# Performance work log

Measured on AMD Instinct MI355X. Metric: run time of the kernel, lower is better.

Reference implementation:

```python
import jax, jax.numpy as jnp
import numpy as np

N_HEAD = 16

def setup_inputs() -> dict:
    key = jax.random.key(0)
    ks = jax.random.split(key, 5)
    B, T, C = 8, 1024, 1024
    s = 0.02
    return {
        "x": jax.random.normal(ks[0], (B, T, C), jnp.float32),
        "W_qkv": jax.random.normal(ks[1], (C, 3 * C), jnp.float32) * s,
        "b_qkv": jnp.zeros((3 * C,), jnp.float32),
        "W_proj": jax.random.normal(ks[2], (C, C), jnp.float32) * s,
        "b_proj": jnp.zeros((C,), jnp.float32),
    }

def reference(x, W_qkv, b_qkv, W_proj, b_proj):
    B, T, C = x.shape
    H = N_HEAD
    hs = C // H
    qkv = x @ W_qkv + b_qkv                       # [B,T,3C]
    q, k, v = jnp.split(qkv, 3, axis=-1)
    # [B,T,C] -> [B,H,T,hs]
    q = q.reshape(B, T, H, hs).transpose(0, 2, 1, 3)
    k = k.reshape(B, T, H, hs).transpose(0, 2, 1, 3)
    v = v.reshape(B, T, H, hs).transpose(0, 2, 1, 3)
    scores = jnp.einsum('bhqd,bhkd->bhqk', q, k) * (hs ** -0.5)  # [B,H,T,T]
    causal = jnp.tril(jnp.ones((T, T), dtype=bool))
    scores = jnp.where(causal[None, None], scores, jnp.finfo(scores.dtype).min)
    attn = jax.nn.softmax(scores, axis=-1)
    # dropout layers are identity in eval mode
    out = jnp.einsum('bhqk,bhkd->bhqd', attn, v)  # [B,H,T,hs]
    out = out.transpose(0, 2, 1, 3).reshape(B, T, C)
    return out @ W_proj + b_proj
```

## Files before the change

### kernel.cpp

```cpp
#include <hip/hip_runtime.h>

#define TT 1024
#define CC 1024
#define NH 16
#define HS 64

typedef __attribute__((ext_vector_type(8))) short short8;
typedef __attribute__((ext_vector_type(4))) float f32x4;

__device__ inline unsigned short f2bf(float f) {
  unsigned int u = __float_as_uint(f);
  unsigned int r = u + 0x7FFFu + ((u >> 16) & 1u);
  return (unsigned short)(r >> 16);
}

__device__ inline unsigned int cvtpk_bf16(float lo, float hi) {
  unsigned int r;
  asm("v_cvt_pk_bf16_f32 %0, %1, %2" : "=v"(r) : "v"(lo), "v"(hi));
  return r;
}

#define GLDS16(g, l)                                                         \
  __builtin_amdgcn_global_load_lds(                                          \
      (const __attribute__((address_space(1))) void*)(g),                    \
      (__attribute__((address_space(3))) void*)(l), 16, 0, 0)

__global__ __launch_bounds__(256) void f32_to_bf16(
    const float* __restrict__ in, unsigned short* __restrict__ out, int n4) {
  int i = (blockIdx.x * 256 + threadIdx.x);
  if (i >= n4) return;
  float4 v = *(const float4*)&in[(size_t)i * 4];
  ushort4 o;
  o.x = f2bf(v.x); o.y = f2bf(v.y); o.z = f2bf(v.z); o.w = f2bf(v.w);
  *(ushort4*)&out[(size_t)i * 4] = o;
}

__global__ __launch_bounds__(256) void transpose_to_bf16(
    const float* __restrict__ W, unsigned short* __restrict__ Wt,
    int K, int N) {
  __shared__ float tile[32][33];
  const int n0 = blockIdx.x * 32, k0 = blockIdx.y * 32;
  const int t = threadIdx.x;
  {
    const int kr = t >> 3;
    const int nc = (t & 7) * 4;
    float4 v = *(const float4*)&W[(size_t)(k0 + kr) * N + n0 + nc];
    tile[kr][nc + 0] = v.x; tile[kr][nc + 1] = v.y;
    tile[kr][nc + 2] = v.z; tile[kr][nc + 3] = v.w;
  }
  __syncthreads();
  {
    const int nr = t >> 3;
    const int kc = (t & 7) * 4;
    ushort4 o;
    o.x = f2bf(tile[kc + 0][nr]);
    o.y = f2bf(tile[kc + 1][nr]);
    o.z = f2bf(tile[kc + 2][nr]);
    o.w = f2bf(tile[kc + 3][nr]);
    *(ushort4*)&Wt[(size_t)(n0 + nr) * K + k0 + kc] = o;
  }
}

template <bool BF16_OUT>
__global__ __launch_bounds__(256) void gemm_bt_mfma(
    const unsigned short* __restrict__ A,
    const unsigned short* __restrict__ Bt,
    const float* __restrict__ bias,
    void* __restrict__ Cv,
    int M, int N, int K) {
  __shared__ __attribute__((aligned(16))) unsigned short As[128 * 32];
  __shared__ __attribute__((aligned(16))) unsigned short Bs[128 * 32];

  const int tid = threadIdx.x;
  const int w = tid >> 6;
  const int l = tid & 63;
  const int wm = w >> 1, wn = w & 1;

  const int brow = blockIdx.y * 128;
  const int bcol = blockIdx.x * 128;

  const int srow = w * 32 + (l >> 2);
  const int skoff = (l & 3) * 8;
  const unsigned short* Ag = A + (size_t)(brow + srow) * K + skoff;
  const unsigned short* Bg = Bt + (size_t)(bcol + srow) * K + skoff;

  typedef __attribute__((address_space(3))) unsigned short lds_us;
  lds_us* AsW = (lds_us*)As + w * 1024;
  lds_us* BsW = (lds_us*)Bs + w * 1024;

  f32x4 acc[4][4] = {};

  const int fr = l & 15;
  const int fk = (l >> 4) * 8;

  const int nk = K >> 5;
  for (int kt = 0; kt < nk; ++kt) {
    const unsigned short* ag = Ag + kt * 32;
    const unsigned short* bg = Bg + kt * 32;
    GLDS16(ag,          AsW);
    GLDS16(ag + 16 * K, AsW + 512);
    GLDS16(bg,          BsW);
    GLDS16(bg + 16 * K, BsW + 512);
    __syncthreads();

    short8 af[4], bfr[4];
#pragma unroll
    for (int m = 0; m < 4; ++m)
      af[m] = *(const short8*)&As[(wm * 64 + m * 16 + fr) * 32 + fk];
#pragma unroll
    for (int n = 0; n < 4; ++n)
      bfr[n] = *(const short8*)&Bs[(wn * 64 + n * 16 + fr) * 32 + fk];
#pragma unroll
    for (int m = 0; m < 4; ++m)
#pragma unroll
      for (int n = 0; n < 4; ++n)
        acc[m][n] = __builtin_amdgcn_mfma_f32_16x16x32_bf16(
            af[m], bfr[n], acc[m][n], 0, 0, 0);
    __syncthreads();
  }

#pragma unroll
  for (int n = 0; n < 4; ++n) {
    const int col = bcol + wn * 64 + n * 16 + fr;
    const float bv = bias[col];
#pragma unroll
    for (int m = 0; m < 4; ++m) {
      const int row0 = brow + wm * 64 + m * 16 + (l >> 4) * 4;
#pragma unroll
      for (int j = 0; j < 4; ++j) {
        const float val = acc[m][n][j] + bv;
        if (BF16_OUT)
          ((unsigned short*)Cv)[(size_t)(row0 + j) * N + col] = f2bf(val);
        else
          ((float*)Cv)[(size_t)(row0 + j) * N + col] = val;
      }
    }
  }
}

#define C1 0.18033688f

__global__ __launch_bounds__(256) void attn_mfma(
    const unsigned short* __restrict__ qkv, unsigned short* __restrict__ aout) {
  const int bh = blockIdx.y;
  const int b = bh >> 4, h = bh & 15;
  const int tid = threadIdx.x;
  const int w = tid >> 6;
  const int l = tid & 63;
  const int lr = l & 15;
  const int lg = l >> 4;

  __shared__ __attribute__((aligned(16))) unsigned short Kl[64 * 64];
  __shared__ __attribute__((aligned(16))) unsigned short Vt[64 * 64];
  __shared__ __attribute__((aligned(16))) unsigned short Pq[4][32 * 64];

  const size_t row3c = 3 * CC;
  const unsigned short* qbase = qkv + (size_t)(b * TT) * row3c + h * HS;
  const unsigned short* kbase = qbase + CC;
  const unsigned short* vbase = qbase + 2 * CC;

  const int ksrow = 16 * w + (l >> 3);
  const int ksbyte = (((l & 7) ^ (l >> 3)) << 4);
  typedef __attribute__((address_space(3))) unsigned short lds_us;
  lds_us* KlW0 = (lds_us*)Kl + (16 * w) * 64;
  lds_us* KlW1 = (lds_us*)Kl + (16 * w + 8) * 64;

#pragma unroll 1
  for (int pass = 0; pass < 2; ++pass) {
    const int qt = pass ? (7 - blockIdx.x) : blockIdx.x;
    const int qw = qt * 128 + w * 32;

    short8 aq[2][2];
#pragma unroll
    for (int mi = 0; mi < 2; ++mi)
#pragma unroll
      for (int ks = 0; ks < 2; ++ks)
        aq[mi][ks] = *(const short8*)(qbase +
            (size_t)(qw + mi * 16 + lr) * row3c + ks * 32 + lg * 8);

    f32x4 sOT[4][2] = {};
    float lpart[2] = {0.f, 0.f};

    const int ntiles = 2 * qt + 2;
    for (int kt = 0; kt < ntiles; ++kt) {
      const int k0 = kt * 64;
      GLDS16((const char*)(kbase + (size_t)(k0 + ksrow) * row3c) + ksbyte, KlW0);
      GLDS16((const char*)(kbase + (size_t)(k0 + 8 + ksrow) * row3c) + ksbyte, KlW1);
      {
        const unsigned short* vsrc = vbase + (size_t)(k0 + l) * row3c + 16 * w;
        short8 v0 = *(const short8*)(vsrc);
        short8 v1 = *(const short8*)(vsrc + 8);
#pragma unroll
        for (int i = 0; i < 8; ++i) {
          const int d0 = 16 * w + i, d1 = d0 + 8;
          Vt[(d0 * 64 + l) ^ ((d0 & 7) << 3)] = (unsigned short)v0[i];
          Vt[(d1 * 64 + l) ^ ((d1 & 7) << 3)] = (unsigned short)v1[i];
        }
      }
      __syncthreads();

      if (k0 <= qw + 31) {
        f32x4 sacc[4][2] = {};
        short8 ak[4][2];
#pragma unroll
        for (int ni = 0; ni < 4; ++ni) {
          const int tok = ni * 16 + lr;
          const int sw = (tok & 7) << 3;
#pragma unroll
          for (int ks = 0; ks < 2; ++ks)
            ak[ni][ks] = *(const short8*)&Kl[tok * 64 + ((ks * 32 + lg * 8) ^ sw)];
        }
#pragma unroll
        for (int ni = 0; ni < 4; ++ni)
#pragma unroll
          for (int mi = 0; mi < 2; ++mi)
#pragma unroll
            for (int ks = 0; ks < 2; ++ks)
              sacc[ni][mi] = __builtin_amdgcn_mfma_f32_16x16x32_bf16(
                  ak[ni][ks], aq[mi][ks], sacc[ni][mi], 0, 0, 0);

        const bool diag = (k0 + 63 > qw);
#pragma unroll
        for (int mi = 0; mi < 2; ++mi) {
          const int qloc = mi * 16 + lr;
          const int qglob = qw + qloc;
          const int psw = (qloc & 7) << 3;
          float ls = 0.f;
#pragma unroll
          for (int ni = 0; ni < 4; ++ni) {
            float p[4];
#pragma unroll
            for (int jj = 0; jj < 4; ++jj) {
              const float pv = exp2f(fmaf(sacc[ni][mi][jj], C1, -2.0f));
              const int kvg = k0 + ni * 16 + lg * 4 + jj;
              p[jj] = (diag && (kvg > qglob)) ? 0.f : pv;
            }
            ls += (p[0] + p[1]) + (p[2] + p[3]);
            uint2 pk;
            pk.x = cvtpk_bf16(p[0], p[1]);
            pk.y = cvtpk_bf16(p[2], p[3]);
            *(uint2*)&Pq[w][qloc * 64 + ((ni * 16 + lg * 4) ^ psw)] = pk;
          }
          lpart[mi] += ls;
        }

        short8 av[4][2], bp[2][2];
#pragma unroll
        for (int nd = 0; nd < 4; ++nd) {
          const int d = nd * 16 + lr;
          const int sw = (d & 7) << 3;
#pragma unroll
          for (int ks = 0; ks < 2; ++ks)
            av[nd][ks] = *(const short8*)&Vt[d * 64 + ((ks * 32 + lg * 8) ^ sw)];
        }
#pragma unroll
        for (int mi = 0; mi < 2; ++mi) {
          const int qloc = mi * 16 + lr;
          const int psw = (qloc & 7) << 3;
#pragma unroll
          for (int ks = 0; ks < 2; ++ks)
            bp[mi][ks] = *(const short8*)&Pq[w][qloc * 64 + ((ks * 32 + lg * 8) ^ psw)];
        }
#pragma unroll
        for (int nd = 0; nd < 4; ++nd)
#pragma unroll
          for (int mi = 0; mi < 2; ++mi)
#pragma unroll
            for (int ks = 0; ks < 2; ++ks)
              sOT[nd][mi] = __builtin_amdgcn_mfma_f32_16x16x32_bf16(
                  av[nd][ks], bp[mi][ks], sOT[nd][mi], 0, 0, 0);
      }
      __syncthreads();
    }

#pragma unroll
    for (int mi = 0; mi < 2; ++mi) {
      float ls = lpart[mi];
      ls += __shfl_xor(ls, 16);
      ls += __shfl_xor(ls, 32);
      const float inv = 1.f / ls;
      const size_t row = (size_t)(b * TT + qw + mi * 16 + lr);
#pragma unroll
      for (int nd = 0; nd < 4; ++nd) {
        uint2 pk;
        pk.x = cvtpk_bf16(sOT[nd][mi][0] * inv, sOT[nd][mi][1] * inv);
        pk.y = cvtpk_bf16(sOT[nd][mi][2] * inv, sOT[nd][mi][3] * inv);
        *(uint2*)&aout[row * CC + h * HS + nd * 16 + lg * 4] = pk;
      }
    }
  }
}

extern "C" void kernel_launch(void* const* d_in, const int* in_sizes, int n_in,
                              void* d_out, int out_size, void* d_ws, size_t ws_size,
                              hipStream_t stream) {
  const float* x     = (const float*)d_in[0];
  const float* Wqkv  = (const float*)d_in[1];
  const float* bqkv  = (const float*)d_in[2];
  const float* Wproj = (const float*)d_in[3];
  const float* bproj = (const float*)d_in[4];
  float* out = (float*)d_out;

  char* ws = (char*)d_ws;
  unsigned short* qkvb   = (unsigned short*)ws;
  unsigned short* xb     = (unsigned short*)(ws + 50331648);
  unsigned short* attnb  = (unsigned short*)(ws + 67108864);
  unsigned short* wqkvt  = (unsigned short*)(ws + 83886080);
  unsigned short* wprojt = (unsigned short*)(ws + 90177536);

  const int M = 8 * TT;

  f32_to_bf16<<<dim3(8192), dim3(256), 0, stream>>>(x, xb, M * CC / 4);
  transpose_to_bf16<<<dim3(96, 32), dim3(256), 0, stream>>>(Wqkv, wqkvt, CC, 3 * CC);
  transpose_to_bf16<<<dim3(32, 32), dim3(256), 0, stream>>>(Wproj, wprojt, CC, CC);

  gemm_bt_mfma<true><<<dim3(3 * CC / 128, M / 128), dim3(256), 0, stream>>>(
      xb, wqkvt, bqkv, qkvb, M, 3 * CC, CC);

  attn_mfma<<<dim3(4, 8 * NH), dim3(256), 0, stream>>>(qkvb, attnb);

  gemm_bt_mfma<false><<<dim3(CC / 128, M / 128), dim3(256), 0, stream>>>(
      attnb, wprojt, bproj, out, M, CC, CC);
}
```

Baseline: 255.1 us.

## Rewrite GEMM with 256x128 tiles, double-buffered LDS, swizzle and XCD remap

Replaces the 128x128 single-buffered GEMM with a 512-thread, 256x128 tile kernel. It double-buffers LDS and prefetches two k-steps ahead with async global-to-LDS loads. It also XOR-swizzles LDS columns to avoid bank conflicts and remaps block IDs across the 8 XCDs for cache locality. The aim is to hide global load latency and raise MFMA utilisation in both projection GEMMs, at the cost of more LDS per block and fragile hand-tuned waitcnt and barrier sequencing.

```diff
diff --git a/kernel.cpp b/kernel.cpp
--- a/kernel.cpp
+++ b/kernel.cpp
@@ -62,73 +62,99 @@
 }
 
 template <bool BF16_OUT>
-__global__ __launch_bounds__(256) void gemm_bt_mfma(
+__global__ __launch_bounds__(512, 4) void gemm_bt_256(
     const unsigned short* __restrict__ A,
     const unsigned short* __restrict__ Bt,
     const float* __restrict__ bias,
     void* __restrict__ Cv,
     int M, int N, int K) {
-  __shared__ __attribute__((aligned(16))) unsigned short As[128 * 32];
-  __shared__ __attribute__((aligned(16))) unsigned short Bs[128 * 32];
+  __shared__ __attribute__((aligned(16))) unsigned short As[2][256 * 32];
+  __shared__ __attribute__((aligned(16))) unsigned short Bs[2][128 * 32];
 
   const int tid = threadIdx.x;
-  const int w = tid >> 6;
-  const int l = tid & 63;
-  const int wm = w >> 1, wn = w & 1;
-
-  const int brow = blockIdx.y * 128;
-  const int bcol = blockIdx.x * 128;
-
-  const int srow = w * 32 + (l >> 2);
-  const int skoff = (l & 3) * 8;
-  const unsigned short* Ag = A + (size_t)(brow + srow) * K + skoff;
-  const unsigned short* Bg = Bt + (size_t)(bcol + srow) * K + skoff;
+  const int w = tid >> 6, l = tid & 63;
+  const int lr = l & 15, lg = l >> 4;
+  const int wr = w >> 1, wc = w & 1;
+
+  const int gx = gridDim.x;
+  const int nwg = gx * gridDim.y;
+  int f = blockIdx.y * gx + blockIdx.x;
+  f = (f & 7) * (nwg >> 3) + (f >> 3);
+  const int bx = f % gx, by = f / gx;
+  const int brow = by * 256, bcol = bx * 128;
+
+  const int ga0 = tid, ga1 = 512 + tid;
+  const int ar0 = ga0 >> 2, ac0 = ga0 & 3;
+  const int ar1 = ga1 >> 2, ac1 = ga1 & 3;
+  const int br_ = tid >> 2, bc_ = tid & 3;
+  const unsigned short* Asrc0 =
+      A + (size_t)(brow + ar0) * K + (ac0 ^ ((ar0 >> 1) & 3)) * 8;
+  const unsigned short* Asrc1 =
+      A + (size_t)(brow + ar1) * K + (ac1 ^ ((ar1 >> 1) & 3)) * 8;
+  const unsigned short* Bsrc =
+      Bt + (size_t)(bcol + br_) * K + (bc_ ^ ((br_ >> 1) & 3)) * 8;
 
   typedef __attribute__((address_space(3))) unsigned short lds_us;
-  lds_us* AsW = (lds_us*)As + w * 1024;
-  lds_us* BsW = (lds_us*)Bs + w * 1024;
+
+#define STAGE(bb, kt)                                                        \
+  do {                                                                       \
+    const int k0_ = (kt) * 32;                                               \
+    GLDS16(Asrc0 + k0_, (lds_us*)&As[bb][0] + ga0 * 8);                      \
+    GLDS16(Asrc1 + k0_, (lds_us*)&As[bb][0] + ga1 * 8);                      \
+    GLDS16(Bsrc + k0_, (lds_us*)&Bs[bb][0] + tid * 8);                       \
+  } while (0)
 
   f32x4 acc[4][4] = {};
 
-  const int fr = l & 15;
-  const int fk = (l >> 4) * 8;
+  const int sfr = ((((lr >> 1) & 3) ^ lg) * 8);
+  const int arow0 = wr * 64 + lr;
+  const int brow0 = wc * 64 + lr;
+
+#define KSTEP(cur, kt, VMASM, DOSTAGE)                                       \
+  do {                                                                       \
+    asm volatile(VMASM ::: "memory");                                        \
+    __builtin_amdgcn_sched_barrier(0);                                       \
+    __builtin_amdgcn_s_barrier();     \
+    short8 af[4], bf[4];                                                     \
+    _Pragma("unroll") for (int mi_ = 0; mi_ < 4; ++mi_)                      \
+        af[mi_] = *(const short8*)&As[cur][(arow0 + mi_ * 16) * 32 + sfr];   \
+    _Pragma("unroll") for (int ni_ = 0; ni_ < 4; ++ni_)                      \
+        bf[ni_] = *(const short8*)&Bs[cur][(brow0 + ni_ * 16) * 32 + sfr];   \
+    asm volatile("s_waitcnt lgkmcnt(0)" ::: "memory");                       \
+    __builtin_amdgcn_sched_barrier(0);                                       \
+    __builtin_amdgcn_s_barrier();          \
+    __builtin_amdgcn_sched_barrier(0);                                       \
+    if (DOSTAGE) STAGE(cur, (kt) + 2);                                       \
+    __builtin_amdgcn_s_setprio(1);                                           \
+    _Pragma("unroll") for (int mi_ = 0; mi_ < 4; ++mi_)                      \
+        _Pragma("unroll") for (int ni_ = 0; ni_ < 4; ++ni_)                  \
+            acc[mi_][ni_] = __builtin_amdgcn_mfma_f32_16x16x32_bf16(         \
+                af[mi_], bf[ni_], acc[mi_][ni_], 0, 0, 0);                   \
+    __builtin_amdgcn_s_setprio(0);                                           \
+  } while (0)
 
   const int nk = K >> 5;
-  for (int kt = 0; kt < nk; ++kt) {
-    const unsigned short* ag = Ag + kt * 32;
-    const unsigned short* bg = Bg + kt * 32;
-    GLDS16(ag,          AsW);
-    GLDS16(ag + 16 * K, AsW + 512);
-    GLDS16(bg,          BsW);
-    GLDS16(bg + 16 * K, BsW + 512);
-    __syncthreads();
-
-    short8 af[4], bfr[4];
-#pragma unroll
-    for (int m = 0; m < 4; ++m)
-      af[m] = *(const short8*)&As[(wm * 64 + m * 16 + fr) * 32 + fk];
-#pragma unroll
-    for (int n = 0; n < 4; ++n)
-      bfr[n] = *(const short8*)&Bs[(wn * 64 + n * 16 + fr) * 32 + fk];
-#pragma unroll
-    for (int m = 0; m < 4; ++m)
-#pragma unroll
-      for (int n = 0; n < 4; ++n)
-        acc[m][n] = __builtin_amdgcn_mfma_f32_16x16x32_bf16(
-            af[m], bfr[n], acc[m][n], 0, 0, 0);
-    __syncthreads();
-  }
-
-#pragma unroll
-  for (int n = 0; n < 4; ++n) {
-    const int col = bcol + wn * 64 + n * 16 + fr;
+  STAGE(0, 0);
+  STAGE(1, 1);
+  int cur = 0;
+  for (int t = 0; t < nk - 1; ++t) {
+    KSTEP(cur, t, "s_waitcnt vmcnt(3)", (t + 2 < nk));
+    cur ^= 1;
+  }
+  KSTEP(cur, nk - 1, "s_waitcnt vmcnt(0)", false);
+#undef KSTEP
+#undef STAGE
+
+#pragma unroll
+  for (int ni = 0; ni < 4; ++ni) {
+    const int col = bcol + wc * 64 + ni * 16 + lr;
     const float bv = bias[col];
 #pragma unroll
-    for (int m = 0; m < 4; ++m) {
-      const int row0 = brow + wm * 64 + m * 16 + (l >> 4) * 4;
+    for (int mi = 0; mi < 4; ++mi) {
+      const int row0 = brow + wr * 64 + mi * 16 + lg * 4;
 #pragma unroll
       for (int j = 0; j < 4; ++j) {
-        const float val = acc[m][n][j] + bv;
+        const float val = acc[mi][ni][j] + bv;
         if (BF16_OUT)
           ((unsigned short*)Cv)[(size_t)(row0 + j) * N + col] = f2bf(val);
         else
@@ -314,11 +340,11 @@
   transpose_to_bf16<<<dim3(96, 32), dim3(256), 0, stream>>>(Wqkv, wqkvt, CC, 3 * CC);
   transpose_to_bf16<<<dim3(32, 32), dim3(256), 0, stream>>>(Wproj, wprojt, CC, CC);
 
-  gemm_bt_mfma<true><<<dim3(3 * CC / 128, M / 128), dim3(256), 0, stream>>>(
+  gemm_bt_256<true><<<dim3(3 * CC / 128, M / 256), dim3(512), 0, stream>>>(
       xb, wqkvt, bqkv, qkvb, M, 3 * CC, CC);
 
   attn_mfma<<<dim3(4, 8 * NH), dim3(256), 0, stream>>>(qkvb, attnb);
 
-  gemm_bt_mfma<false><<<dim3(CC / 128, M / 128), dim3(256), 0, stream>>>(
+  gemm_bt_256<false><<<dim3(CC / 128, M / 256), dim3(512), 0, stream>>>(
       attnb, wprojt, bproj, out, M, CC, CC);
 }
```

Measured after the change: 244.1 us. 4.3% less time.
